# Kernel optimization log

Measured on AMD Instinct MI355X. Metric: run time of the kernel, lower is better.

## Reference

```python
import jax, jax.numpy as jnp
import numpy as np

N = 50000   # nodes
E = 800000  # edges
D = 128     # input feature dim
H = 128     # hidden dim
L = 3       # num GIN layers
G = 64      # graphs in batch


def setup_inputs() -> dict:
    key = jax.random.key(0)
    ks = jax.random.split(key, 20)
    inp = {
        "h": jax.random.normal(ks[0], (N, D), jnp.float32),
        "src": jax.random.randint(ks[1], (E,), 0, N),
        "dst": jax.random.randint(ks[2], (E,), 0, N),
        "graph_ids": jnp.sort(jax.random.randint(ks[3], (N,), 0, G)),
    }
    k = 4
    for i in range(L):
        in_dim = D if i == 0 else H
        inp[f"w1_{i}"] = jax.random.normal(ks[k], (in_dim, H), jnp.float32) / np.sqrt(in_dim).astype(np.float32); k += 1
        inp[f"b1_{i}"] = jnp.zeros((H,), jnp.float32)
        inp[f"w2_{i}"] = jax.random.normal(ks[k], (H, H), jnp.float32) / np.sqrt(H).astype(np.float32); k += 1
        inp[f"b2_{i}"] = jnp.zeros((H,), jnp.float32)
    inp["w_out"] = jax.random.normal(ks[k], (H * L, 1), jnp.float32) / np.sqrt(H * L).astype(np.float32)
    inp["b_out"] = jnp.zeros((1,), jnp.float32)
    return inp


def _gin_layer(h, src, dst, w1, b1, w2, b2):
    # sum aggregation over edges: agg[i] = sum_{(j->i) in E} h[j]
    agg = jax.ops.segment_sum(h[src], dst, num_segments=N)
    z = h + agg  # (1 + eps) * h + agg with eps = 0 (DGL GINConv default)
    return jax.nn.relu(z @ w1 + b1) @ w2 + b2  # 2-layer MLP


def reference(h, src, dst, graph_ids,
              w1_0, b1_0, w2_0, b2_0,
              w1_1, b1_1, w2_1, b2_1,
              w1_2, b1_2, w2_2, b2_2,
              w_out, b_out):
    layers = [(w1_0, b1_0, w2_0, b2_0),
              (w1_1, b1_1, w2_1, b2_1),
              (w1_2, b1_2, w2_2, b2_2)]
    readouts = []
    for w1, b1, w2, b2 in layers:
        h = _gin_layer(h, src, dst, w1, b1, w2, b2)
        # per-graph sum readout of node features: [G, H]
        readouts.append(jax.ops.segment_sum(h, graph_ids, num_segments=G))
    hg = jnp.concatenate(readouts, axis=1)  # [G, H*L]
    return hg @ w_out + b_out  # [G, 1]
```

## Files before the change

### kernel.cpp

```cpp
#include <hip/hip_runtime.h>

#define NN 50000
#define NE 800000
#define DIMH 128
#define NGRAPH 64
#define NTILES 3125
#define PAIRS 1024
#define MLP_BLOCKS 512
#define MLP_ITERS 4
#define NBIN 196
#define BCAP 8064
#define SL_US 800000
#define SL_U4 100000

typedef __attribute__((ext_vector_type(8))) short bf16x8;
typedef __attribute__((ext_vector_type(4))) float f32x4;

__device__ __forceinline__ unsigned short f2b(float f) {
  unsigned int b = __float_as_uint(f);
  unsigned int r = (b + 0x7FFFu + ((b >> 16) & 1u)) >> 16;
  return (unsigned short)r;
}
__device__ __forceinline__ float b2f_lo(unsigned int u) { return __uint_as_float(u << 16); }
__device__ __forceinline__ float b2f_hi(unsigned int u) { return __uint_as_float(u & 0xffff0000u); }
__device__ __forceinline__ unsigned int pk2(float lo, float hi) {
  return (unsigned int)f2b(lo) | ((unsigned int)f2b(hi) << 16);
}
__device__ __forceinline__ void add8(float* a, uint4 u) {
  a[0] += b2f_lo(u.x); a[1] += b2f_hi(u.x);
  a[2] += b2f_lo(u.y); a[3] += b2f_hi(u.y);
  a[4] += b2f_lo(u.z); a[5] += b2f_hi(u.z);
  a[6] += b2f_lo(u.w); a[7] += b2f_hi(u.w);
}


__global__ __launch_bounds__(256) void bin_scatter_kernel(const int* __restrict__ src,
                                                          const int* __restrict__ dst,
                                                          int* __restrict__ gcnt,
                                                          int2* __restrict__ staging) {
  __shared__ int hist[NBIN];
  __shared__ int base[NBIN];
  int tid = threadIdx.x;
  for (int i = tid; i < NBIN; i += 256) hist[i] = 0;
  __syncthreads();
  int e0 = blockIdx.x * 2048;
  int2 ed[8];
  int bin[8], rank[8];
#pragma unroll
  for (int k = 0; k < 8; ++k) {
    int e = e0 + k * 256 + tid;
    bin[k] = 0; rank[k] = 0; ed[k] = make_int2(0, 0);
    if (e < NE) {
      ed[k].x = src[e]; ed[k].y = dst[e];
      bin[k] = ed[k].y >> 8;
      rank[k] = atomicAdd(&hist[bin[k]], 1);
    }
  }
  __syncthreads();
  for (int i = tid; i < NBIN; i += 256) base[i] = atomicAdd(&gcnt[i], hist[i]);
  __syncthreads();
#pragma unroll
  for (int k = 0; k < 8; ++k) {
    int e = e0 + k * 256 + tid;
    if (e < NE) staging[bin[k] * BCAP + base[bin[k]] + rank[k]] = ed[k];
  }
}

__global__ __launch_bounds__(256) void bin_fill_kernel(const int2* __restrict__ staging,
                                                       const int* __restrict__ gcnt,
                                                       int* __restrict__ adj,
                                                       int* __restrict__ row_ptr,
                                                       int* __restrict__ cnt,
                                                       int* __restrict__ alloc) {
  __shared__ int hdeg[256], loc[256], c2[256];
  __shared__ int sbase;
  int b = blockIdx.x;
  int tid = threadIdx.x;
  hdeg[tid] = 0; c2[tid] = 0;
  __syncthreads();
  int n = gcnt[b];
  for (int i = tid; i < n; i += 256)
    atomicAdd(&hdeg[staging[b * BCAP + i].y & 255], 1);
  __syncthreads();
  int v = hdeg[tid];
  int va = (v + 1) & ~1;
  loc[tid] = va;
  __syncthreads();
  for (int off = 1; off < 256; off <<= 1) {
    int t = (tid >= off) ? loc[tid - off] : 0;
    __syncthreads();
    loc[tid] += t;
    __syncthreads();
  }
  if (tid == 255) sbase = atomicAdd(alloc, loc[255]);
  __syncthreads();
  int excl = loc[tid] - va;
  int node = b * 256 + tid;
  if (node < NN) { row_ptr[node] = sbase + excl; cnt[node] = v; }
  loc[tid] = excl;
  __syncthreads();
  for (int i = tid; i < n; i += 256) {
    int2 e = staging[b * BCAP + i];
    int local = e.y & 255;
    int r = atomicAdd(&c2[local], 1);
    adj[sbase + loc[local] + r] = e.x;
  }
}


struct WPtrs { const float* w[6]; const float* b_out; const float* b2_last;
               const float* w_out; };

__global__ __launch_bounds__(256) void prep_kernel(WPtrs ptrs, unsigned short* __restrict__ wt,
                                                   float* __restrict__ out,
                                                   int* __restrict__ gcnt,
                                                   int* __restrict__ alloc,
                                                   float* __restrict__ v2,
                                                   float* __restrict__ s2) {
  int i = blockIdx.x * 256 + threadIdx.x;
  int m = i >> 14;
  int idx = i & 16383;
  int c = idx >> 7, k = idx & 127;
  wt[m * 16384 + idx] = f2b(ptrs.w[m][k * DIMH + c]);
  if (i < NGRAPH) out[i] = ptrs.b_out[0];
  if (i < NBIN) gcnt[i] = 0;
  if (i == NBIN) *alloc = 0;
  if (i < DIMH) {
    const float* w2r = ptrs.w[5] + i * DIMH;
    const float* wo = ptrs.w_out + 2 * DIMH;
    float s0 = 0.f, s1 = 0.f, sa = 0.f, sb = 0.f;
#pragma unroll 4
    for (int cc = 0; cc < DIMH; cc += 4) {
      s0 += w2r[cc] * wo[cc];
      s1 += w2r[cc + 1] * wo[cc + 1];
      sa += w2r[cc + 2] * wo[cc + 2];
      sb += w2r[cc + 3] * wo[cc + 3];
    }
    v2[i] = (s0 + s1) + (sa + sb);
  }
  if (i == DIMH) {
    const float* wo = ptrs.w_out + 2 * DIMH;
    float s0 = 0.f, s1 = 0.f, sa = 0.f, sb = 0.f;
#pragma unroll 4
    for (int cc = 0; cc < DIMH; cc += 4) {
      s0 += ptrs.b2_last[cc] * wo[cc];
      s1 += ptrs.b2_last[cc + 1] * wo[cc + 1];
      sa += ptrs.b2_last[cc + 2] * wo[cc + 2];
      sb += ptrs.b2_last[cc + 3] * wo[cc + 3];
    }
    *s2 = (s0 + s1) + (sa + sb);
  }
}

__global__ void convh_kernel(const float* __restrict__ h, uint2* __restrict__ Hs) {
  int t = blockIdx.x * 256 + threadIdx.x;
  if (t >= NN * 32) return;
  int node = t >> 5;
  int q = t & 31;
  float4 v = *(const float4*)&h[node * DIMH + q * 4];
  uint2 o;
  o.x = pk2(v.x, v.y);
  o.y = pk2(v.z, v.w);
  Hs[(q >> 2) * (SL_U4 * 2) + node * 4 + (q & 3)] = o;
}

__global__ __launch_bounds__(256) void agg_kernel(const uint4* __restrict__ Hs,
                                                  const int* __restrict__ row_ptr,
                                                  const int* __restrict__ cnt,
                                                  const int* __restrict__ adj,
                                                  uint4* __restrict__ Zs) {
  int bid = blockIdx.x;
  int slice = bid & 7;
  int nb = bid >> 3;
  int tid = threadIdx.x;
  int node = nb * 128 + (tid >> 1);
  int l2 = tid & 1;
  if (node >= NN) return;
  const uint4* hp = Hs + slice * SL_U4;
  int start = row_ptr[node];
  int c = cnt[node];
  float a[8];
  {
    uint4 own = hp[node * 2 + l2];
    a[0] = b2f_lo(own.x); a[1] = b2f_hi(own.x);
    a[2] = b2f_lo(own.y); a[3] = b2f_hi(own.y);
    a[4] = b2f_lo(own.z); a[5] = b2f_hi(own.z);
    a[6] = b2f_lo(own.w); a[7] = b2f_hi(own.w);
  }
  int j = 0;
  for (; j + 8 <= c; j += 8) {
    int2 i01 = *(const int2*)(adj + start + j);
    int2 i23 = *(const int2*)(adj + start + j + 2);
    int2 i45 = *(const int2*)(adj + start + j + 4);
    int2 i67 = *(const int2*)(adj + start + j + 6);
    uint4 u0 = hp[i01.x * 2 + l2];
    uint4 u1 = hp[i01.y * 2 + l2];
    uint4 u2 = hp[i23.x * 2 + l2];
    uint4 u3 = hp[i23.y * 2 + l2];
    uint4 u4 = hp[i45.x * 2 + l2];
    uint4 u5 = hp[i45.y * 2 + l2];
    uint4 u6 = hp[i67.x * 2 + l2];
    uint4 u7 = hp[i67.y * 2 + l2];
    add8(a, u0); add8(a, u1); add8(a, u2); add8(a, u3);
    add8(a, u4); add8(a, u5); add8(a, u6); add8(a, u7);
  }
  for (; j + 2 <= c; j += 2) {
    int2 i01 = *(const int2*)(adj + start + j);
    uint4 u0 = hp[i01.x * 2 + l2];
    uint4 u1 = hp[i01.y * 2 + l2];
    add8(a, u0); add8(a, u1);
  }
  if (j < c) {
    int n0 = adj[start + j];
    add8(a, hp[n0 * 2 + l2]);
  }
  uint4 o;
  o.x = pk2(a[0], a[1]);
  o.y = pk2(a[2], a[3]);
  o.z = pk2(a[4], a[5]);
  o.w = pk2(a[6], a[7]);
  Zs[slice * SL_U4 + node * 2 + l2] = o;
}

__global__ __launch_bounds__(256, 2) void mlp_mid_kernel(const unsigned short* __restrict__ X,
                                                         const unsigned short* __restrict__ W1t,
                                                         const float* __restrict__ b1,
                                                         const unsigned short* __restrict__ W2t,
                                                         const float* __restrict__ b2,
                                                         unsigned short* __restrict__ Y,
                                                         const int* __restrict__ gids,
                                                         const float* __restrict__ wout,
                                                         float* __restrict__ gout) {
  __shared__ unsigned short y1[2][2][2048];
  __shared__ float s_gout[NGRAPH];
  int tid = threadIdx.x;
  if (tid < NGRAPH) s_gout[tid] = 0.f;

  int wv = tid >> 6;
  int lane = tid & 63;
  int pb = wv >> 1;
  int half = wv & 1;
  int l15 = lane & 15;
  int g = lane >> 4;
  int p = blockIdx.x * 2 + pb;

  int asl_base = (g >> 1) * SL_US + (g & 1) * 8 + l15 * 16;

  bf16x8 a[4];
  {
    int roff = p * 256;
#pragma unroll
    for (int kt = 0; kt < 4; ++kt)
      a[kt] = *(const bf16x8*)(X + 2 * kt * SL_US + roff + asl_base);
  }

  bf16x8 fb1[4][4], fb2[4][4];
  const unsigned short* w1b = W1t + (half * 64 + l15) * DIMH + g * 8;
  const unsigned short* w2b = W2t + (half * 64 + l15) * DIMH + g * 8;
#pragma unroll
  for (int n = 0; n < 4; ++n)
#pragma unroll
    for (int kt = 0; kt < 4; ++kt) {
      fb1[n][kt] = *(const bf16x8*)(w1b + n * 16 * DIMH + kt * 32);
      fb2[n][kt] = *(const bf16x8*)(w2b + n * 16 * DIMH + kt * 32);
    }
  float b1v[4], b2v[4], wov[4];
#pragma unroll
  for (int n = 0; n < 4; ++n) {
    int col = half * 64 + n * 16 + l15;
    b1v[n] = b1[col];
    b2v[n] = b2[col];
    wov[n] = wout[col];
  }
  __syncthreads();

#pragma unroll
  for (int i = 0; i < MLP_ITERS; ++i) {
    int rtc = p + i * PAIRS;
    bool active = rtc < NTILES;
    unsigned short* buf = y1[pb][i & 1];

    if (active) {
#pragma unroll
      for (int n = 0; n < 4; ++n) {
        f32x4 acc = (f32x4){0.f, 0.f, 0.f, 0.f};
#pragma unroll
        for (int kt = 0; kt < 4; ++kt)
          acc = __builtin_amdgcn_mfma_f32_16x16x32_bf16(a[kt], fb1[n][kt], acc, 0, 0, 0);
        int col2 = (half * 64 + n * 16 + l15) * 2;
#pragma unroll
        for (int r = 0; r < 4; ++r) {
          float f = fmaxf(acc[r] + b1v[n], 0.f);
          int row = 4 * g + r;
          buf[((row * 256 + col2) ^ (row << 4)) >> 1] = f2b(f);
        }
      }
    }

    int rtn = p + (i + 1) * PAIRS;
    if (i + 1 < MLP_ITERS && rtn < NTILES) {
      int roff = rtn * 256;
#pragma unroll
      for (int kt = 0; kt < 4; ++kt)
        a[kt] = *(const bf16x8*)(X + 2 * kt * SL_US + roff + asl_base);
    }

    __syncthreads();

    if (active) {
      bf16x8 a2[4];
#pragma unroll
      for (int kt = 0; kt < 4; ++kt)
        a2[kt] = *(const bf16x8*)&buf[((l15 * 256 + kt * 64 + g * 16) ^ (l15 << 4)) >> 1];

      float pr[4] = {0.f, 0.f, 0.f, 0.f};
#pragma unroll
      for (int n = 0; n < 4; ++n) {
        f32x4 acc = (f32x4){0.f, 0.f, 0.f, 0.f};
#pragma unroll
        for (int kt = 0; kt < 4; ++kt)
          acc = __builtin_amdgcn_mfma_f32_16x16x32_bf16(a2[kt], fb2[n][kt], acc, 0, 0, 0);
        int sl = 4 * half + n;
#pragma unroll
        for (int r = 0; r < 4; ++r) {
          float f = acc[r] + b2v[n];
          Y[sl * SL_US + (rtc * 16 + 4 * g + r) * 16 + l15] = f2b(f);
          pr[r] += f * wov[n];
        }
      }
#pragma unroll
      for (int r = 0; r < 4; ++r) {
#pragma unroll
        for (int off = 1; off < 16; off <<= 1) pr[r] += __shfl_xor(pr[r], off, 64);
      }
      if (l15 == 0) {
#pragma unroll
        for (int r = 0; r < 4; ++r)
          atomicAdd(&s_gout[gids[rtc * 16 + 4 * g + r]], pr[r]);
      }
    }
  }

  __syncthreads();
  if (tid < NGRAPH) {
    float v = s_gout[tid];
    if (v != 0.f) atomicAdd(&gout[tid], v);
  }
}

__global__ __launch_bounds__(256, 2) void mlp_last_kernel(const unsigned short* __restrict__ X,
                                                          const unsigned short* __restrict__ W1t,
                                                          const float* __restrict__ b1,
                                                          const int* __restrict__ gids,
                                                          float* __restrict__ gout,
                                                          const float* __restrict__ v2,
                                                          const float* __restrict__ s2p) {
  __shared__ float s_gout[NGRAPH];
  int tid = threadIdx.x;
  if (tid < NGRAPH) s_gout[tid] = 0.f;

  int wv = tid >> 6;
  int lane = tid & 63;
  int half = wv & 1;
  int pbase = blockIdx.x * 2 + (wv >> 1);
  int l15 = lane & 15;
  int g = lane >> 4;

  int asl_base = (g >> 1) * SL_US + (g & 1) * 8 + l15 * 16;

  bf16x8 fb1[4][4];
  const unsigned short* w1b = W1t + (half * 64 + l15) * DIMH + g * 8;
#pragma unroll
  for (int n = 0; n < 4; ++n)
#pragma unroll
    for (int kt = 0; kt < 4; ++kt)
      fb1[n][kt] = *(const bf16x8*)(w1b + n * 16 * DIMH + kt * 32);
  float b1v[4], v2v[4];
#pragma unroll
  for (int n = 0; n < 4; ++n) {
    int col = half * 64 + n * 16 + l15;
    b1v[n] = b1[col];
    v2v[n] = v2[col];
  }
  float s2v = (half == 0) ? *s2p : 0.f;
  __syncthreads();

  bf16x8 a[4];
  {
    int roff = pbase * 256;
#pragma unroll
    for (int kt = 0; kt < 4; ++kt)
      a[kt] = *(const bf16x8*)(X + 2 * kt * SL_US + roff + asl_base);
  }

#pragma unroll
  for (int i = 0; i < MLP_ITERS; ++i) {
    int rtc = pbase + i * PAIRS;
    bool active = rtc < NTILES;

    bf16x8 cur[4];
#pragma unroll
    for (int kt = 0; kt < 4; ++kt) cur[kt] = a[kt];

    int rtn = pbase + (i + 1) * PAIRS;
    if (i + 1 < MLP_ITERS && rtn < NTILES) {
      int roff = rtn * 256;
#pragma unroll
      for (int kt = 0; kt < 4; ++kt)
        a[kt] = *(const bf16x8*)(X + 2 * kt * SL_US + roff + asl_base);
    }

    if (active) {
      float pr[4] = {0.f, 0.f, 0.f, 0.f};
#pragma unroll
      for (int n = 0; n < 4; ++n) {
        f32x4 acc = (f32x4){0.f, 0.f, 0.f, 0.f};
#pragma unroll
        for (int kt = 0; kt < 4; ++kt)
          acc = __builtin_amdgcn_mfma_f32_16x16x32_bf16(cur[kt], fb1[n][kt], acc, 0, 0, 0);
#pragma unroll
        for (int r = 0; r < 4; ++r)
          pr[r] += fmaxf(acc[r] + b1v[n], 0.f) * v2v[n];
      }
#pragma unroll
      for (int r = 0; r < 4; ++r) {
#pragma unroll
        for (int off = 1; off < 16; off <<= 1) pr[r] += __shfl_xor(pr[r], off, 64);
      }
      if (l15 == 0) {
#pragma unroll
        for (int r = 0; r < 4; ++r)
          atomicAdd(&s_gout[gids[rtc * 16 + 4 * g + r]], pr[r] + s2v);
      }
    }
  }

  __syncthreads();
  if (tid < NGRAPH) {
    float v = s_gout[tid];
    if (v != 0.f) atomicAdd(&gout[tid], v);
  }
}


extern "C" void kernel_launch(void* const* d_in, const int* in_sizes, int n_in,
                              void* d_out, int out_size, void* d_ws, size_t ws_size,
                              hipStream_t stream) {
  const float* h = (const float*)d_in[0];
  const int* src = (const int*)d_in[1];
  const int* dst = (const int*)d_in[2];
  const int* gids = (const int*)d_in[3];
  const float* w_out = (const float*)d_in[16];
  const float* b_out = (const float*)d_in[17];
  float* out = (float*)d_out;

  char* base = (char*)d_ws;
  unsigned short* buf0 = (unsigned short*)(base);
  unsigned short* buf1 = (unsigned short*)(base + 12800000);
  int2* staging = (int2*)(base + 25600000);
  int* adj = (int*)(base + 38400000);
  int* row_ptr = (int*)(base + 41800064);
  int* cnt = (int*)(base + 42000128);
  int* gcnt = (int*)(base + 42200192);
  int* alloc = (int*)(base + 42201024);
  unsigned short* wt = (unsigned short*)(base + 42201088);
  float* v2 = (float*)(base + 42397696);
  float* s2 = (float*)(base + 42398208);
  unsigned short* Zs = (unsigned short*)(base + 42400000);

  WPtrs ptrs;
  for (int l = 0; l < 3; ++l) {
    ptrs.w[2 * l] = (const float*)d_in[4 + l * 4];
    ptrs.w[2 * l + 1] = (const float*)d_in[6 + l * 4];
  }
  ptrs.b_out = b_out;
  ptrs.b2_last = (const float*)d_in[15];
  ptrs.w_out = w_out;

  prep_kernel<<<384, 256, 0, stream>>>(ptrs, wt, out, gcnt, alloc, v2, s2);
  bin_scatter_kernel<<<(NE + 2047) / 2048, 256, 0, stream>>>(src, dst, gcnt, staging);
  bin_fill_kernel<<<NBIN, 256, 0, stream>>>(staging, gcnt, adj, row_ptr, cnt, alloc);
  convh_kernel<<<(NN * 32 + 255) / 256, 256, 0, stream>>>(h, (uint2*)buf0);

  int agg_blocks = 391 * 8;

  for (int l = 0; l < 3; ++l) {
    const float* b1 = (const float*)d_in[5 + l * 4];
    const float* b2 = (const float*)d_in[7 + l * 4];
    const unsigned short* Hl = (l & 1) ? buf1 : buf0;
    unsigned short* Yl = (l & 1) ? buf0 : buf1;
    agg_kernel<<<agg_blocks, 256, 0, stream>>>((const uint4*)Hl, row_ptr, cnt, adj,
                                               (uint4*)Zs);
    if (l < 2) {
      mlp_mid_kernel<<<MLP_BLOCKS, 256, 0, stream>>>(Zs, wt + (2 * l) * 16384, b1,
                                                     wt + (2 * l + 1) * 16384, b2,
                                                     Yl, gids, w_out + l * DIMH, out);
    } else {
      mlp_last_kernel<<<MLP_BLOCKS, 256, 0, stream>>>(Zs, wt + (2 * l) * 16384, b1,
                                                      gids, out, v2, s2);
    }
  }
}
```

Baseline: 215.2 us.

## Store node features in fp32 and split fused MLP into separate GEMM kernels

Node features, aggregation buffers and layer outputs are kept in fp32 instead of packed bf16, with conversion to bf16 done only when loading MFMA operands. The fused two-GEMM MLP kernel, which staged the hidden activation in shared memory, is replaced by separate gemm1 and gemm2 kernels that pass the hidden activation through a global fp32 buffer. The persistent multi-tile loop is replaced by one tile per wave. This roughly doubles gather and store bandwidth and adds a kernel launch plus an intermediate round trip, in exchange for simpler code and higher intermediate precision.

```diff
diff --git a/kernel.cpp b/kernel.cpp
--- a/kernel.cpp
+++ b/kernel.cpp
@@ -5,13 +5,10 @@
 #define DIMH 128
 #define NGRAPH 64
 #define NTILES 3125
-#define PAIRS 1024
-#define MLP_BLOCKS 512
-#define MLP_ITERS 4
+#define GEMM_BLOCKS 1563
 #define NBIN 196
 #define BCAP 8064
-#define SL_US 800000
-#define SL_U4 100000
+#define SL_F 800000
 
 typedef __attribute__((ext_vector_type(8))) short bf16x8;
 typedef __attribute__((ext_vector_type(4))) float f32x4;
@@ -21,16 +18,16 @@
   unsigned int r = (b + 0x7FFFu + ((b >> 16) & 1u)) >> 16;
   return (unsigned short)r;
 }
-__device__ __forceinline__ float b2f_lo(unsigned int u) { return __uint_as_float(u << 16); }
-__device__ __forceinline__ float b2f_hi(unsigned int u) { return __uint_as_float(u & 0xffff0000u); }
-__device__ __forceinline__ unsigned int pk2(float lo, float hi) {
-  return (unsigned int)f2b(lo) | ((unsigned int)f2b(hi) << 16);
-}
-__device__ __forceinline__ void add8(float* a, uint4 u) {
-  a[0] += b2f_lo(u.x); a[1] += b2f_hi(u.x);
-  a[2] += b2f_lo(u.y); a[3] += b2f_hi(u.y);
-  a[4] += b2f_lo(u.z); a[5] += b2f_hi(u.z);
-  a[6] += b2f_lo(u.w); a[7] += b2f_hi(u.w);
+
+__device__ __forceinline__ bf16x8 ld8(const float* p) {
+  float4 v0 = *(const float4*)p;
+  float4 v1 = *(const float4*)(p + 4);
+  bf16x8 r;
+  r[0] = (short)f2b(v0.x); r[1] = (short)f2b(v0.y);
+  r[2] = (short)f2b(v0.z); r[3] = (short)f2b(v0.w);
+  r[4] = (short)f2b(v1.x); r[5] = (short)f2b(v1.y);
+  r[6] = (short)f2b(v1.z); r[7] = (short)f2b(v1.w);
+  return r;
 }
 
 
@@ -152,192 +149,178 @@
   }
 }
 
-__global__ void convh_kernel(const float* __restrict__ h, uint2* __restrict__ Hs) {
+__global__ void convh_kernel(const float* __restrict__ h, float4* __restrict__ Hs) {
   int t = blockIdx.x * 256 + threadIdx.x;
   if (t >= NN * 32) return;
   int node = t >> 5;
   int q = t & 31;
   float4 v = *(const float4*)&h[node * DIMH + q * 4];
-  uint2 o;
-  o.x = pk2(v.x, v.y);
-  o.y = pk2(v.z, v.w);
-  Hs[(q >> 2) * (SL_U4 * 2) + node * 4 + (q & 3)] = o;
-}
-
-__global__ __launch_bounds__(256) void agg_kernel(const uint4* __restrict__ Hs,
+  Hs[(q >> 2) * (SL_F / 4) + node * 4 + (q & 3)] = v;
+}
+
+__global__ __launch_bounds__(256) void agg_kernel(const float4* __restrict__ Hs,
                                                   const int* __restrict__ row_ptr,
                                                   const int* __restrict__ cnt,
                                                   const int* __restrict__ adj,
-                                                  uint4* __restrict__ Zs) {
+                                                  float4* __restrict__ Zs) {
   int bid = blockIdx.x;
   int slice = bid & 7;
   int nb = bid >> 3;
   int tid = threadIdx.x;
-  int node = nb * 128 + (tid >> 1);
-  int l2 = tid & 1;
+  int node = nb * 64 + (tid >> 2);
+  int l4 = tid & 3;
   if (node >= NN) return;
-  const uint4* hp = Hs + slice * SL_U4;
+  const float4* hp = Hs + slice * (SL_F / 4);
   int start = row_ptr[node];
   int c = cnt[node];
-  float a[8];
-  {
-    uint4 own = hp[node * 2 + l2];
-    a[0] = b2f_lo(own.x); a[1] = b2f_hi(own.x);
-    a[2] = b2f_lo(own.y); a[3] = b2f_hi(own.y);
-    a[4] = b2f_lo(own.z); a[5] = b2f_hi(own.z);
-    a[6] = b2f_lo(own.w); a[7] = b2f_hi(own.w);
-  }
+  float4 own = hp[node * 4 + l4];
+  float a0 = own.x, a1 = own.y, a2 = own.z, a3 = own.w;
   int j = 0;
   for (; j + 8 <= c; j += 8) {
     int2 i01 = *(const int2*)(adj + start + j);
     int2 i23 = *(const int2*)(adj + start + j + 2);
     int2 i45 = *(const int2*)(adj + start + j + 4);
     int2 i67 = *(const int2*)(adj + start + j + 6);
-    uint4 u0 = hp[i01.x * 2 + l2];
-    uint4 u1 = hp[i01.y * 2 + l2];
-    uint4 u2 = hp[i23.x * 2 + l2];
-    uint4 u3 = hp[i23.y * 2 + l2];
-    uint4 u4 = hp[i45.x * 2 + l2];
-    uint4 u5 = hp[i45.y * 2 + l2];
-    uint4 u6 = hp[i67.x * 2 + l2];
-    uint4 u7 = hp[i67.y * 2 + l2];
-    add8(a, u0); add8(a, u1); add8(a, u2); add8(a, u3);
-    add8(a, u4); add8(a, u5); add8(a, u6); add8(a, u7);
+    float4 u0 = hp[i01.x * 4 + l4];
+    float4 u1 = hp[i01.y * 4 + l4];
+    float4 u2 = hp[i23.x * 4 + l4];
+    float4 u3 = hp[i23.y * 4 + l4];
+    float4 u4 = hp[i45.x * 4 + l4];
+    float4 u5 = hp[i45.y * 4 + l4];
+    float4 u6 = hp[i67.x * 4 + l4];
+    float4 u7 = hp[i67.y * 4 + l4];
+    a0 += u0.x; a1 += u0.y; a2 += u0.z; a3 += u0.w;
+    a0 += u1.x; a1 += u1.y; a2 += u1.z; a3 += u1.w;
+    a0 += u2.x; a1 += u2.y; a2 += u2.z; a3 += u2.w;
+    a0 += u3.x; a1 += u3.y; a2 += u3.z; a3 += u3.w;
+    a0 += u4.x; a1 += u4.y; a2 += u4.z; a3 += u4.w;
+    a0 += u5.x; a1 += u5.y; a2 += u5.z; a3 += u5.w;
+    a0 += u6.x; a1 += u6.y; a2 += u6.z; a3 += u6.w;
+    a0 += u7.x; a1 += u7.y; a2 += u7.z; a3 += u7.w;
   }
   for (; j + 2 <= c; j += 2) {
     int2 i01 = *(const int2*)(adj + start + j);
-    uint4 u0 = hp[i01.x * 2 + l2];
-    uint4 u1 = hp[i01.y * 2 + l2];
-    add8(a, u0); add8(a, u1);
+    float4 u0 = hp[i01.x * 4 + l4];
+    float4 u1 = hp[i01.y * 4 + l4];
+    a0 += u0.x; a1 += u0.y; a2 += u0.z; a3 += u0.w;
+    a0 += u1.x; a1 += u1.y; a2 += u1.z; a3 += u1.w;
   }
   if (j < c) {
-    int n0 = adj[start + j];
-    add8(a, hp[n0 * 2 + l2]);
-  }
-  uint4 o;
-  o.x = pk2(a[0], a[1]);
-  o.y = pk2(a[2], a[3]);
-  o.z = pk2(a[4], a[5]);
-  o.w = pk2(a[6], a[7]);
-  Zs[slice * SL_U4 + node * 2 + l2] = o;
-}
-
-__global__ __launch_bounds__(256, 2) void mlp_mid_kernel(const unsigned short* __restrict__ X,
-                                                         const unsigned short* __restrict__ W1t,
-                                                         const float* __restrict__ b1,
-                                                         const unsigned short* __restrict__ W2t,
-                                                         const float* __restrict__ b2,
-                                                         unsigned short* __restrict__ Y,
-                                                         const int* __restrict__ gids,
-                                                         const float* __restrict__ wout,
-                                                         float* __restrict__ gout) {
-  __shared__ unsigned short y1[2][2][2048];
-  __shared__ float s_gout[NGRAPH];
-  int tid = threadIdx.x;
-  if (tid < NGRAPH) s_gout[tid] = 0.f;
-
-  int wv = tid >> 6;
+    float4 u = hp[adj[start + j] * 4 + l4];
+    a0 += u.x; a1 += u.y; a2 += u.z; a3 += u.w;
+  }
+  Zs[slice * (SL_F / 4) + node * 4 + l4] = make_float4(a0, a1, a2, a3);
+}
+
+
+__global__ __launch_bounds__(256) void gemm1_kernel(const float* __restrict__ X,
+                                                    const unsigned short* __restrict__ W1t,
+                                                    const float* __restrict__ b1,
+                                                    float* __restrict__ Y1) {
+  int tid = threadIdx.x;
+  int gw = blockIdx.x * 4 + (tid >> 6);
   int lane = tid & 63;
-  int pb = wv >> 1;
-  int half = wv & 1;
+  int half = gw & 1;
+  int rt = gw >> 1;
+  if (rt >= NTILES) return;
   int l15 = lane & 15;
   int g = lane >> 4;
-  int p = blockIdx.x * 2 + pb;
-
-  int asl_base = (g >> 1) * SL_US + (g & 1) * 8 + l15 * 16;
+  const float* xp = X + (g >> 1) * SL_F + (g & 1) * 8 + (rt * 16 + l15) * 16;
 
   bf16x8 a[4];
-  {
-    int roff = p * 256;
+#pragma unroll
+  for (int kt = 0; kt < 4; ++kt) a[kt] = ld8(xp + 2 * kt * SL_F);
+
+  bf16x8 fb[4][4];
+  const unsigned short* wb = W1t + (half * 64 + l15) * DIMH + g * 8;
+#pragma unroll
+  for (int n = 0; n < 4; ++n)
 #pragma unroll
     for (int kt = 0; kt < 4; ++kt)
-      a[kt] = *(const bf16x8*)(X + 2 * kt * SL_US + roff + asl_base);
-  }
-
-  bf16x8 fb1[4][4], fb2[4][4];
-  const unsigned short* w1b = W1t + (half * 64 + l15) * DIMH + g * 8;
-  const unsigned short* w2b = W2t + (half * 64 + l15) * DIMH + g * 8;
-#pragma unroll
-  for (int n = 0; n < 4; ++n)
-#pragma unroll
-    for (int kt = 0; kt < 4; ++kt) {
-      fb1[n][kt] = *(const bf16x8*)(w1b + n * 16 * DIMH + kt * 32);
-      fb2[n][kt] = *(const bf16x8*)(w2b + n * 16 * DIMH + kt * 32);
-    }
-  float b1v[4], b2v[4], wov[4];
+      fb[n][kt] = *(const bf16x8*)(wb + n * 16 * DIMH + kt * 32);
+  float bv[4];
+#pragma unroll
+  for (int n = 0; n < 4; ++n) bv[n] = b1[half * 64 + n * 16 + l15];
+
 #pragma unroll
   for (int n = 0; n < 4; ++n) {
-    int col = half * 64 + n * 16 + l15;
-    b1v[n] = b1[col];
-    b2v[n] = b2[col];
-    wov[n] = wout[col];
-  }
-  __syncthreads();
-
-#pragma unroll
-  for (int i = 0; i < MLP_ITERS; ++i) {
-    int rtc = p + i * PAIRS;
-    bool active = rtc < NTILES;
-    unsigned short* buf = y1[pb][i & 1];
-
-    if (active) {
-#pragma unroll
-      for (int n = 0; n < 4; ++n) {
-        f32x4 acc = (f32x4){0.f, 0.f, 0.f, 0.f};
-#pragma unroll
-        for (int kt = 0; kt < 4; ++kt)
-          acc = __builtin_amdgcn_mfma_f32_16x16x32_bf16(a[kt], fb1[n][kt], acc, 0, 0, 0);
-        int col2 = (half * 64 + n * 16 + l15) * 2;
-#pragma unroll
-        for (int r = 0; r < 4; ++r) {
-          float f = fmaxf(acc[r] + b1v[n], 0.f);
-          int row = 4 * g + r;
-          buf[((row * 256 + col2) ^ (row << 4)) >> 1] = f2b(f);
-        }
+    f32x4 acc = (f32x4){0.f, 0.f, 0.f, 0.f};
+#pragma unroll
+    for (int kt = 0; kt < 4; ++kt)
+      acc = __builtin_amdgcn_mfma_f32_16x16x32_bf16(a[kt], fb[n][kt], acc, 0, 0, 0);
+    int sl = 4 * half + n;
+#pragma unroll
+    for (int r = 0; r < 4; ++r) {
+      float f = fmaxf(acc[r] + bv[n], 0.f);
+      Y1[sl * SL_F + (rt * 16 + 4 * g + r) * 16 + l15] = f;
+    }
+  }
+}
+
+__global__ __launch_bounds__(256) void gemm2_kernel(const float* __restrict__ X,
+                                                    const unsigned short* __restrict__ W2t,
+                                                    const float* __restrict__ b2,
+                                                    float* __restrict__ Y,
+                                                    const int* __restrict__ gids,
+                                                    const float* __restrict__ wout,
+                                                    float* __restrict__ gout) {
+  __shared__ float s_gout[NGRAPH];
+  int tid = threadIdx.x;
+  if (tid < NGRAPH) s_gout[tid] = 0.f;
+  __syncthreads();
+
+  int gw = blockIdx.x * 4 + (tid >> 6);
+  int lane = tid & 63;
+  int half = gw & 1;
+  int rt = gw >> 1;
+  int l15 = lane & 15;
+  int g = lane >> 4;
+
+  if (rt < NTILES) {
+    const float* xp = X + (g >> 1) * SL_F + (g & 1) * 8 + (rt * 16 + l15) * 16;
+    bf16x8 a[4];
+#pragma unroll
+    for (int kt = 0; kt < 4; ++kt) a[kt] = ld8(xp + 2 * kt * SL_F);
+
+    bf16x8 fb[4][4];
+    const unsigned short* wb = W2t + (half * 64 + l15) * DIMH + g * 8;
+#pragma unroll
+    for (int n = 0; n < 4; ++n)
+#pragma unroll
+      for (int kt = 0; kt < 4; ++kt)
+        fb[n][kt] = *(const bf16x8*)(wb + n * 16 * DIMH + kt * 32);
+    float bv[4], wov[4];
+#pragma unroll
+    for (int n = 0; n < 4; ++n) {
+      int col = half * 64 + n * 16 + l15;
+      bv[n] = b2[col];
+      wov[n] = wout[col];
+    }
+
+    float pr[4] = {0.f, 0.f, 0.f, 0.f};
+#pragma unroll
+    for (int n = 0; n < 4; ++n) {
+      f32x4 acc = (f32x4){0.f, 0.f, 0.f, 0.f};
+#pragma unroll
+      for (int kt = 0; kt < 4; ++kt)
+        acc = __builtin_amdgcn_mfma_f32_16x16x32_bf16(a[kt], fb[n][kt], acc, 0, 0, 0);
+      int sl = 4 * half + n;
+#pragma unroll
+      for (int r = 0; r < 4; ++r) {
+        float f = acc[r] + bv[n];
+        Y[sl * SL_F + (rt * 16 + 4 * g + r) * 16 + l15] = f;
+        pr[r] += f * wov[n];
       }
     }
-
-    int rtn = p + (i + 1) * PAIRS;
-    if (i + 1 < MLP_ITERS && rtn < NTILES) {
-      int roff = rtn * 256;
-#pragma unroll
-      for (int kt = 0; kt < 4; ++kt)
-        a[kt] = *(const bf16x8*)(X + 2 * kt * SL_US + roff + asl_base);
-    }
-
-    __syncthreads();
-
-    if (active) {
-      bf16x8 a2[4];
-#pragma unroll
-      for (int kt = 0; kt < 4; ++kt)
-        a2[kt] = *(const bf16x8*)&buf[((l15 * 256 + kt * 64 + g * 16) ^ (l15 << 4)) >> 1];
-
-      float pr[4] = {0.f, 0.f, 0.f, 0.f};
-#pragma unroll
-      for (int n = 0; n < 4; ++n) {
-        f32x4 acc = (f32x4){0.f, 0.f, 0.f, 0.f};
-#pragma unroll
-        for (int kt = 0; kt < 4; ++kt)
-          acc = __builtin_amdgcn_mfma_f32_16x16x32_bf16(a2[kt], fb2[n][kt], acc, 0, 0, 0);
-        int sl = 4 * half + n;
-#pragma unroll
-        for (int r = 0; r < 4; ++r) {
-          float f = acc[r] + b2v[n];
-          Y[sl * SL_US + (rtc * 16 + 4 * g + r) * 16 + l15] = f2b(f);
-          pr[r] += f * wov[n];
-        }
-      }
-#pragma unroll
-      for (int r = 0; r < 4; ++r) {
-#pragma unroll
-        for (int off = 1; off < 16; off <<= 1) pr[r] += __shfl_xor(pr[r], off, 64);
-      }
-      if (l15 == 0) {
-#pragma unroll
-        for (int r = 0; r < 4; ++r)
-          atomicAdd(&s_gout[gids[rtc * 16 + 4 * g + r]], pr[r]);
-      }
+#pragma unroll
+    for (int r = 0; r < 4; ++r) {
+#pragma unroll
+      for (int off = 1; off < 16; off <<= 1) pr[r] += __shfl_xor(pr[r], off, 64);
+    }
+    if (l15 == 0) {
+#pragma unroll
+      for (int r = 0; r < 4; ++r)
+        atomicAdd(&s_gout[gids[rt * 16 + 4 * g + r]], pr[r]);
     }
   }
 
@@ -348,90 +331,67 @@
   }
 }
 
-__global__ __launch_bounds__(256, 2) void mlp_last_kernel(const unsigned short* __restrict__ X,
-                                                          const unsigned short* __restrict__ W1t,
-                                                          const float* __restrict__ b1,
-                                                          const int* __restrict__ gids,
-                                                          float* __restrict__ gout,
-                                                          const float* __restrict__ v2,
-                                                          const float* __restrict__ s2p) {
+__global__ __launch_bounds__(256) void gemm_last_kernel(const float* __restrict__ X,
+                                                        const unsigned short* __restrict__ W1t,
+                                                        const float* __restrict__ b1,
+                                                        const int* __restrict__ gids,
+                                                        float* __restrict__ gout,
+                                                        const float* __restrict__ v2,
+                                                        const float* __restrict__ s2p) {
   __shared__ float s_gout[NGRAPH];
   int tid = threadIdx.x;
   if (tid < NGRAPH) s_gout[tid] = 0.f;
-
-  int wv = tid >> 6;
+  __syncthreads();
+
+  int gw = blockIdx.x * 4 + (tid >> 6);
   int lane = tid & 63;
-  int half = wv & 1;
-  int pbase = blockIdx.x * 2 + (wv >> 1);
+  int half = gw & 1;
+  int rt = gw >> 1;
   int l15 = lane & 15;
   int g = lane >> 4;
 
-  int asl_base = (g >> 1) * SL_US + (g & 1) * 8 + l15 * 16;
-
-  bf16x8 fb1[4][4];
-  const unsigned short* w1b = W1t + (half * 64 + l15) * DIMH + g * 8;
-#pragma unroll
-  for (int n = 0; n < 4; ++n)
-#pragma unroll
-    for (int kt = 0; kt < 4; ++kt)
-      fb1[n][kt] = *(const bf16x8*)(w1b + n * 16 * DIMH + kt * 32);
-  float b1v[4], v2v[4];
-#pragma unroll
-  for (int n = 0; n < 4; ++n) {
-    int col = half * 64 + n * 16 + l15;
-    b1v[n] = b1[col];
-    v2v[n] = v2[col];
-  }
-  float s2v = (half == 0) ? *s2p : 0.f;
-  __syncthreads();
-
-  bf16x8 a[4];
-  {
-    int roff = pbase * 256;
-#pragma unroll
-    for (int kt = 0; kt < 4; ++kt)
-      a[kt] = *(const bf16x8*)(X + 2 * kt * SL_US + roff + asl_base);
-  }
-
-#pragma unroll
-  for (int i = 0; i < MLP_ITERS; ++i) {
-    int rtc = pbase + i * PAIRS;
-    bool active = rtc < NTILES;
-
-    bf16x8 cur[4];
-#pragma unroll
-    for (int kt = 0; kt < 4; ++kt) cur[kt] = a[kt];
-
-    int rtn = pbase + (i + 1) * PAIRS;
-    if (i + 1 < MLP_ITERS && rtn < NTILES) {
-      int roff = rtn * 256;
+  if (rt < NTILES) {
+    const float* xp = X + (g >> 1) * SL_F + (g & 1) * 8 + (rt * 16 + l15) * 16;
+    bf16x8 a[4];
+#pragma unroll
+    for (int kt = 0; kt < 4; ++kt) a[kt] = ld8(xp + 2 * kt * SL_F);
+
+    bf16x8 fb[4][4];
+    const unsigned short* wb = W1t + (half * 64 + l15) * DIMH + g * 8;
+#pragma unroll
+    for (int n = 0; n < 4; ++n)
 #pragma unroll
       for (int kt = 0; kt < 4; ++kt)
-        a[kt] = *(const bf16x8*)(X + 2 * kt * SL_US + roff + asl_base);
-    }
-
-    if (active) {
-      float pr[4] = {0.f, 0.f, 0.f, 0.f};
-#pragma unroll
-      for (int n = 0; n < 4; ++n) {
-        f32x4 acc = (f32x4){0.f, 0.f, 0.f, 0.f};
-#pragma unroll
-        for (int kt = 0; kt < 4; ++kt)
-          acc = __builtin_amdgcn_mfma_f32_16x16x32_bf16(cur[kt], fb1[n][kt], acc, 0, 0, 0);
-#pragma unroll
-        for (int r = 0; r < 4; ++r)
-          pr[r] += fmaxf(acc[r] + b1v[n], 0.f) * v2v[n];
-      }
-#pragma unroll
-      for (int r = 0; r < 4; ++r) {
-#pragma unroll
-        for (int off = 1; off < 16; off <<= 1) pr[r] += __shfl_xor(pr[r], off, 64);
-      }
-      if (l15 == 0) {
-#pragma unroll
-        for (int r = 0; r < 4; ++r)
-          atomicAdd(&s_gout[gids[rtc * 16 + 4 * g + r]], pr[r] + s2v);
-      }
+        fb[n][kt] = *(const bf16x8*)(wb + n * 16 * DIMH + kt * 32);
+    float bv[4], v2v[4];
+#pragma unroll
+    for (int n = 0; n < 4; ++n) {
+      int col = half * 64 + n * 16 + l15;
+      bv[n] = b1[col];
+      v2v[n] = v2[col];
+    }
+    float s2v = (half == 0) ? *s2p : 0.f;
+
+    float pr[4] = {0.f, 0.f, 0.f, 0.f};
+#pragma unroll
+    for (int n = 0; n < 4; ++n) {
+      f32x4 acc = (f32x4){0.f, 0.f, 0.f, 0.f};
+#pragma unroll
+      for (int kt = 0; kt < 4; ++kt)
+        acc = __builtin_amdgcn_mfma_f32_16x16x32_bf16(a[kt], fb[n][kt], acc, 0, 0, 0);
+#pragma unroll
+      for (int r = 0; r < 4; ++r)
+        pr[r] += fmaxf(acc[r] + bv[n], 0.f) * v2v[n];
+    }
+#pragma unroll
+    for (int r = 0; r < 4; ++r) {
+#pragma unroll
+      for (int off = 1; off < 16; off <<= 1) pr[r] += __shfl_xor(pr[r], off, 64);
+    }
+    if (l15 == 0) {
+#pragma unroll
+      for (int r = 0; r < 4; ++r)
+        atomicAdd(&s_gout[gids[rt * 16 + 4 * g + r]], pr[r] + s2v);
     }
   }
 
@@ -455,18 +415,19 @@
   float* out = (float*)d_out;
 
   char* base = (char*)d_ws;
-  unsigned short* buf0 = (unsigned short*)(base);
-  unsigned short* buf1 = (unsigned short*)(base + 12800000);
-  int2* staging = (int2*)(base + 25600000);
-  int* adj = (int*)(base + 38400000);
-  int* row_ptr = (int*)(base + 41800064);
-  int* cnt = (int*)(base + 42000128);
-  int* gcnt = (int*)(base + 42200192);
-  int* alloc = (int*)(base + 42201024);
-  unsigned short* wt = (unsigned short*)(base + 42201088);
-  float* v2 = (float*)(base + 42397696);
-  float* s2 = (float*)(base + 42398208);
-  unsigned short* Zs = (unsigned short*)(base + 42400000);
+  float* buf0 = (float*)(base);
+  float* buf1 = (float*)(base + 25600000);
+  float* Zs   = (float*)(base + 51200000);
+  float* Y1   = (float*)(base + 76800000);
+  int2* staging = (int2*)(base + 102400000);
+  int* adj = (int*)(base + 115200000);
+  int* row_ptr = (int*)(base + 118600064);
+  int* cnt = (int*)(base + 118800128);
+  int* gcnt = (int*)(base + 119000192);
+  int* alloc = (int*)(base + 119001024);
+  unsigned short* wt = (unsigned short*)(base + 119002048);
+  float* v2 = (float*)(base + 119198720);
+  float* s2 = (float*)(base + 119199232);
 
   WPtrs ptrs;
   for (int l = 0; l < 3; ++l) {
@@ -480,24 +441,24 @@
   prep_kernel<<<384, 256, 0, stream>>>(ptrs, wt, out, gcnt, alloc, v2, s2);
   bin_scatter_kernel<<<(NE + 2047) / 2048, 256, 0, stream>>>(src, dst, gcnt, staging);
   bin_fill_kernel<<<NBIN, 256, 0, stream>>>(staging, gcnt, adj, row_ptr, cnt, alloc);
-  convh_kernel<<<(NN * 32 + 255) / 256, 256, 0, stream>>>(h, (uint2*)buf0);
-
-  int agg_blocks = 391 * 8;
+  convh_kernel<<<(NN * 32 + 255) / 256, 256, 0, stream>>>(h, (float4*)buf0);
+
+  int agg_blocks = 782 * 8;
 
   for (int l = 0; l < 3; ++l) {
     const float* b1 = (const float*)d_in[5 + l * 4];
     const float* b2 = (const float*)d_in[7 + l * 4];
-    const unsigned short* Hl = (l & 1) ? buf1 : buf0;
-    unsigned short* Yl = (l & 1) ? buf0 : buf1;
-    agg_kernel<<<agg_blocks, 256, 0, stream>>>((const uint4*)Hl, row_ptr, cnt, adj,
-                                               (uint4*)Zs);
+    const float* Hl = (l & 1) ? buf1 : buf0;
+    float* Yl = (l & 1) ? buf0 : buf1;
+    agg_kernel<<<agg_blocks, 256, 0, stream>>>((const float4*)Hl, row_ptr, cnt, adj,
+                                               (float4*)Zs);
     if (l < 2) {
-      mlp_mid_kernel<<<MLP_BLOCKS, 256, 0, stream>>>(Zs, wt + (2 * l) * 16384, b1,
-                                                     wt + (2 * l + 1) * 16384, b2,
-                                                     Yl, gids, w_out + l * DIMH, out);
+      gemm1_kernel<<<GEMM_BLOCKS, 256, 0, stream>>>(Zs, wt + (2 * l) * 16384, b1, Y1);
+      gemm2_kernel<<<GEMM_BLOCKS, 256, 0, stream>>>(Y1, wt + (2 * l + 1) * 16384, b2,
+                                                    Yl, gids, w_out + l * DIMH, out);
     } else {
-      mlp_last_kernel<<<MLP_BLOCKS, 256, 0, stream>>>(Zs, wt + (2 * l) * 16384, b1,
-                                                      gids, out, v2, s2);
-    }
-  }
-}
+      gemm_last_kernel<<<GEMM_BLOCKS, 256, 0, stream>>>(Zs, wt + (2 * l) * 16384, b1,
+                                                        gids, out, v2, s2);
+    }
+  }
+}
```

After: 291.6 us. 35.5% more time.
